# Kernel optimization log

Hardware: AMD Instinct MI355X
Metric: run time of the kernel (lower is better)

## Reference

```python
import jax, jax.numpy as jnp
import numpy as np

N, K, H = 50000, 8, 128  # nodes per level, mailbox fanout, hidden size


def setup_inputs() -> dict:
    key = jax.random.key(0)
    ks = jax.random.split(key, 16)
    s = 1.0 / np.sqrt(H)
    inp = {
        "x": jax.random.normal(ks[0], (N, H), jnp.float32),
        "h_mail": jax.random.normal(ks[1], (N, K, H), jnp.float32),
        "c_mail": jax.random.normal(ks[2], (N, K, H), jnp.float32),
        "Wiou": jax.random.uniform(ks[3], (H, 3 * H), jnp.float32, -s, s),
        "Uiou": jax.random.uniform(ks[4], (2 * H, 3 * H), jnp.float32, -s, s),
        "biou": jnp.zeros((1, 3 * H), jnp.float32),
        "Of": jax.random.uniform(ks[5], (H, H), jnp.float32, -s, s),
        "Zf": jax.random.uniform(ks[6], (H, H), jnp.float32, -s, s),
        "Qf": jax.random.uniform(ks[7], (H, H), jnp.float32, -s, s),
        "Kf": jax.random.uniform(ks[8], (H, H), jnp.float32, -s, s),
        "vf": jax.random.uniform(ks[9], (H, H), jnp.float32, -s, s),
        "Wa": jax.random.uniform(ks[10], (H, H), jnp.float32, -s, s),
        "Wd": jax.random.uniform(ks[11], (H, H), jnp.float32, -s, s),
        "Vf": jax.random.uniform(ks[12], (H, 1), jnp.float32, -s, s),
        "etype": jax.random.randint(ks[13], (N, K), 0, 2, jnp.int32),
    }
    return inp


def reference(x, h_mail, c_mail, Wiou, Uiou, biou, Of, Zf, Qf, Kf, vf, Wa, Wd, Vf, etype):
    # --- message: mailbox of child h, c and edge type e (0/1) ---
    e = etype.astype(x.dtype)[..., None]                     # [N,K,1]
    # --- reduce_func ---
    x_tild = x @ Wiou                                        # W_iou(features) -> iou  [N,3H]
    n_tild = x @ Qf                                          # [N,H]
    hk = h_mail @ Kf                                         # K_f(h_tild) [N,K,H]
    v_tild = hk @ vf                                         # [N,K,H]
    w = jax.nn.softmax(jnp.tanh((n_tild[:, None, :] + hk) @ Vf), axis=1)  # [N,K,1]
    modify = jnp.mean(e, axis=1)                             # sum(et)/K  [N,1]
    score_a = (1.0 - modify)[:, None, :]                     # [N,1,1]
    score_b = modify[:, None, :]
    h_til1 = jnp.sum(w * score_a * e * (v_tild @ Wa), axis=1)        # [N,H]
    h_til0 = jnp.sum(w * score_b * (1.0 - e) * (v_tild @ Wd), axis=1)
    h_tild = jnp.concatenate([h_til0, h_til1], axis=1)       # [N,2H]
    f = jax.nn.sigmoid((h_mail * e) @ Of + (h_mail * (1.0 - e)) @ Zf)
    c_red = jnp.sum(f * c_mail, axis=1)                      # [N,H]
    iou = h_tild @ Uiou + x_tild                             # [N,3H]
    # --- apply_node_func ---
    iou = iou + biou
    i, o, u = jnp.split(iou, 3, axis=1)
    i, o, u = jax.nn.sigmoid(i), jax.nn.sigmoid(o), jnp.tanh(u)
    c = i * u + c_red
    h = o * jnp.tanh(c)
    return jnp.stack([h, c])                                 # [2,N,H]
```

## Files before the change

kernel.cpp:

```cpp
#include <hip/hip_runtime.h>
#include <math.h>

#define NN 50000
#define HH 128
#define KK 8

#define WS_WTF  0
#define WS_BT   16384
#define WS_KV   90112
#define WS_T0   106496
#define WS_T1   122880
#define WS_kv   139264
#define WS_qv   139392

typedef __attribute__((ext_vector_type(8))) unsigned short u16x8;
typedef __attribute__((ext_vector_type(8))) __bf16 bf16x8;
typedef __attribute__((ext_vector_type(4))) float f32x4;
union Frag { u16x8 u; bf16x8 b; };

__device__ __forceinline__ unsigned short f2bf(float f) {
    unsigned u = __builtin_bit_cast(unsigned, f);
    u += 0x7fffu + ((u >> 16) & 1u);
    return (unsigned short)(u >> 16);
}
__device__ __forceinline__ float sigm(float v) { return 1.f / (1.f + expf(-v)); }

__global__ void prep1(const float* __restrict__ Kf, const float* __restrict__ Qf,
                      const float* __restrict__ vf, const float* __restrict__ Vf,
                      const float* __restrict__ Wiou, float* __restrict__ ws) {
    int idx = blockIdx.x * 256 + threadIdx.x;
    unsigned short* bt = (unsigned short*)(ws + WS_BT);
    if (idx < 16384) {
        int a = idx >> 7, c = idx & 127;
        float s = 0.f;
        for (int b = 0; b < 128; ++b) s += Kf[a * 128 + b] * vf[b * 128 + c];
        ws[WS_KV + idx] = s;
    } else if (idx < 16512) {
        int a = idx - 16384;
        float s = 0.f;
        for (int b = 0; b < 128; ++b) s += Kf[a * 128 + b] * Vf[b];
        ws[WS_kv + a] = s;
    } else if (idx < 16640) {
        int a = idx - 16512;
        float s = 0.f;
        for (int b = 0; b < 128; ++b) s += Qf[a * 128 + b] * Vf[b];
        ws[WS_qv + a] = s;
    } else {
        int i = idx - 16640;
        int r = i / 384, c = i % 384;
        bt[c * 384 + r] = f2bf(Wiou[i]);
    }
}

__global__ void prep2(const float* __restrict__ Wd, const float* __restrict__ Wa,
                      float* __restrict__ ws) {
    int idx = blockIdx.x * 256 + threadIdx.x;
    int sel = idx >> 14;
    int r = (idx >> 7) & 127, c = idx & 127;
    const float* W = sel ? Wa : Wd;
    const float* Kv = ws + WS_KV;
    float s = 0.f;
    for (int h = 0; h < 128; ++h) s += Kv[r * 128 + h] * W[h * 128 + c];
    ws[(sel ? WS_T1 : WS_T0) + r * 128 + c] = s;
}

__global__ void prep3(const float* __restrict__ Uiou, float* __restrict__ ws) {
    int idx = blockIdx.x * 256 + threadIdx.x;
    int half = (idx >= 49152) ? 1 : 0;
    int i2 = idx - half * 49152;
    int r = i2 / 384, c = i2 % 384;
    const float* T = ws + (half ? WS_T1 : WS_T0);
    const float* U = Uiou + half * 128 * 384;
    float s = 0.f;
    for (int h = 0; h < 128; ++h) s += T[r * 128 + h] * U[h * 384 + c];
    unsigned short* bt = (unsigned short*)(ws + WS_BT);
    bt[c * 384 + (128 + half * 128 + r)] = f2bf(s);
}

__global__ void prep4(const float* __restrict__ Of, const float* __restrict__ Zf,
                      float* __restrict__ ws) {
    int idx = blockIdx.x * 256 + threadIdx.x;
    int c = idx >> 8, k = idx & 255;
    float v = (k < 128) ? Of[k * 128 + c] : Zf[(k - 128) * 128 + c];
    unsigned short* wtf = (unsigned short*)(ws + WS_WTF);
    wtf[idx] = f2bf(v);
}

__global__ __launch_bounds__(256) void tree_main(
    const float* __restrict__ x, const float* __restrict__ h_mail,
    const float* __restrict__ c_mail, const float* __restrict__ biou,
    const int* __restrict__ etype, const float* __restrict__ ws,
    float* __restrict__ out)
{
    __shared__ unsigned short GfS[48 * 128];
    __shared__ float credS[16 * 128];
    __shared__ float iouS[16 * 388];
    __shared__ float efS[128];
    __shared__ float kvqS[256];

    const int t = threadIdx.x;
    const int node0 = blockIdx.x * 16;

    {
        const int n = t >> 4, s = t & 15, c0 = s * 8;
        const int node = node0 + n;
        kvqS[t] = ws[WS_kv + t];
        if (t < 128) efS[t] = (float)etype[node0 * KK + t];

        float xv[8];
        const float4* xp = (const float4*)(x + node * HH + c0);
        float4 x0 = xp[0], x1 = xp[1];
        xv[0]=x0.x; xv[1]=x0.y; xv[2]=x0.z; xv[3]=x0.w;
        xv[4]=x1.x; xv[5]=x1.y; xv[6]=x1.z; xv[7]=x1.w;
        u16x8 xg;
        #pragma unroll
        for (int j = 0; j < 8; ++j) xg[j] = f2bf(xv[j]);
        *(u16x8*)(&GfS[s * 128 + n * 8]) = xg;
        __syncthreads();

        float xq = 0.f;
        #pragma unroll
        for (int j = 0; j < 8; ++j) xq += xv[j] * kvqS[128 + c0 + j];

        float p[KK];
        #pragma unroll
        for (int k = 0; k < KK; ++k) {
            const float4* hp = (const float4*)(h_mail + (node * KK + k) * HH + c0);
            float4 h0 = hp[0], h1 = hp[1];
            p[k] = h0.x*kvqS[c0]   + h0.y*kvqS[c0+1] + h0.z*kvqS[c0+2] + h0.w*kvqS[c0+3]
                 + h1.x*kvqS[c0+4] + h1.y*kvqS[c0+5] + h1.z*kvqS[c0+6] + h1.w*kvqS[c0+7];
        }
        #pragma unroll
        for (int msk = 8; msk >= 1; msk >>= 1) {
            xq += __shfl_xor(xq, msk, 16);
            #pragma unroll
            for (int k = 0; k < KK; ++k) p[k] += __shfl_xor(p[k], msk, 16);
        }
        float ef[KK], esum = 0.f;
        #pragma unroll
        for (int k = 0; k < KK; ++k) { ef[k] = efS[n * KK + k]; esum += ef[k]; }
        const float mod = esum * 0.125f;
        const float sa = 1.f - mod, sb = mod;

        float tk[KK], mx = -1e30f;
        #pragma unroll
        for (int k = 0; k < KK; ++k) { tk[k] = tanhf(xq + p[k]); mx = fmaxf(mx, tk[k]); }
        float wsum = 0.f;
        #pragma unroll
        for (int k = 0; k < KK; ++k) { tk[k] = expf(tk[k] - mx); wsum += tk[k]; }
        const float inv = 1.f / wsum;
        float cf0[KK], cf1[KK];
        #pragma unroll
        for (int k = 0; k < KK; ++k) {
            float w = tk[k] * inv;
            cf0[k] = sb * w * (1.f - ef[k]);
            cf1[k] = sa * w * ef[k];
        }
        float a0[8] = {0,0,0,0,0,0,0,0}, a1[8] = {0,0,0,0,0,0,0,0};
        #pragma unroll
        for (int k = 0; k < KK; ++k) {
            const float4* hp = (const float4*)(h_mail + (node * KK + k) * HH + c0);
            float4 h0 = hp[0], h1 = hp[1];
            float hv[8];
            hv[0]=h0.x; hv[1]=h0.y; hv[2]=h0.z; hv[3]=h0.w;
            hv[4]=h1.x; hv[5]=h1.y; hv[6]=h1.z; hv[7]=h1.w;
            #pragma unroll
            for (int j = 0; j < 8; ++j) { a0[j] += cf0[k]*hv[j]; a1[j] += cf1[k]*hv[j]; }
        }
        u16x8 g0, g1;
        #pragma unroll
        for (int j = 0; j < 8; ++j) { g0[j] = f2bf(a0[j]); g1[j] = f2bf(a1[j]); }
        *(u16x8*)(&GfS[(16 + s) * 128 + n * 8]) = g0;
        *(u16x8*)(&GfS[(32 + s) * 128 + n * 8]) = g1;
    }
    __syncthreads();

    const int wave = t >> 6, lane = t & 63, m = lane & 15, q = lane >> 4;
    {
        const unsigned short* WtF = (const unsigned short*)(ws + WS_WTF);
        f32x4 acc[2][8];
        #pragma unroll
        for (int rt = 0; rt < 2; ++rt)
            #pragma unroll
            for (int tc = 0; tc < 8; ++tc) acc[rt][tc] = (f32x4){0.f,0.f,0.f,0.f};

        #pragma unroll
        for (int ks = 0; ks < 8; ++ks) {
            const int kg = ks * 32 + q * 8;
            Frag bf[8], af[2];
            #pragma unroll
            for (int tc = 0; tc < 8; ++tc)
                bf[tc].u = *(const u16x8*)(WtF + (tc * 16 + m) * 256 + kg);
            #pragma unroll
            for (int rt = 0; rt < 2; ++rt) {
                const int r = wave * 32 + rt * 16 + m;
                const float msk = (ks < 4) ? efS[r] : (1.f - efS[r]);
                const float4* hp = (const float4*)(h_mail + (node0 * KK + r) * HH + (kg & 127));
                float4 h0 = hp[0], h1 = hp[1];
                float tv[8];
                tv[0]=h0.x*msk; tv[1]=h0.y*msk; tv[2]=h0.z*msk; tv[3]=h0.w*msk;
                tv[4]=h1.x*msk; tv[5]=h1.y*msk; tv[6]=h1.z*msk; tv[7]=h1.w*msk;
                #pragma unroll
                for (int j = 0; j < 8; ++j) af[rt].u[j] = f2bf(tv[j]);
            }
            #pragma unroll
            for (int rt = 0; rt < 2; ++rt)
                #pragma unroll
                for (int tc = 0; tc < 8; ++tc)
                    acc[rt][tc] = __builtin_amdgcn_mfma_f32_16x16x32_bf16(
                        af[rt].b, bf[tc].b, acc[rt][tc], 0, 0, 0);
        }
        #pragma unroll
        for (int rt = 0; rt < 2; ++rt) {
            const int rbase = wave * 32 + rt * 16;
            #pragma unroll
            for (int tc = 0; tc < 8; ++tc) {
                float sacc = 0.f;
                #pragma unroll
                for (int reg = 0; reg < 4; ++reg) {
                    const int r = rbase + q * 4 + reg;
                    const float f = sigm(acc[rt][tc][reg]);
                    sacc += f * c_mail[(node0 * KK + r) * HH + tc * 16 + m];
                }
                sacc += __shfl_xor(sacc, 16);
                if ((q & 1) == 0) {
                    const int nl = (rbase >> 3) + (q >> 1);
                    credS[nl * 128 + tc * 16 + m] = sacc;
                }
            }
        }
    }

    {
        const unsigned short* Bt = (const unsigned short*)(ws + WS_BT);
        f32x4 acc2[6];
        #pragma unroll
        for (int j = 0; j < 6; ++j) acc2[j] = (f32x4){0.f,0.f,0.f,0.f};
        #pragma unroll
        for (int ks = 0; ks < 12; ++ks) {
            const int kg = ks * 32 + q * 8;
            Frag ag;
            ag.u = *(const u16x8*)(&GfS[(kg >> 3) * 128 + m * 8]);
            #pragma unroll
            for (int j = 0; j < 6; ++j) {
                const int tc = wave * 6 + j;
                Frag bg;
                bg.u = *(const u16x8*)(Bt + (tc * 16 + m) * 384 + kg);
                acc2[j] = __builtin_amdgcn_mfma_f32_16x16x32_bf16(
                    ag.b, bg.b, acc2[j], 0, 0, 0);
            }
        }
        #pragma unroll
        for (int j = 0; j < 6; ++j) {
            const int tc = wave * 6 + j;
            #pragma unroll
            for (int reg = 0; reg < 4; ++reg)
                iouS[(q * 4 + reg) * 388 + tc * 16 + m] = acc2[j][reg];
        }
    }
    __syncthreads();

    {
        const int n = t >> 4, s = t & 15, c0 = s * 8;
        const int node = node0 + n;
        float hb[8], cb[8];
        #pragma unroll
        for (int j = 0; j < 8; ++j) {
            const int c = c0 + j;
            const float ii = sigm(iouS[n * 388 + c] + biou[c]);
            const float oo = sigm(iouS[n * 388 + 128 + c] + biou[128 + c]);
            const float uu = tanhf(iouS[n * 388 + 256 + c] + biou[256 + c]);
            const float cc = ii * uu + credS[n * 128 + c];
            cb[j] = cc;
            hb[j] = oo * tanhf(cc);
        }
        float4* oh = (float4*)(out + node * HH + c0);
        oh[0] = make_float4(hb[0], hb[1], hb[2], hb[3]);
        oh[1] = make_float4(hb[4], hb[5], hb[6], hb[7]);
        float4* oc = (float4*)(out + NN * HH + node * HH + c0);
        oc[0] = make_float4(cb[0], cb[1], cb[2], cb[3]);
        oc[1] = make_float4(cb[4], cb[5], cb[6], cb[7]);
    }
}

extern "C" void kernel_launch(void* const* d_in, const int* in_sizes, int n_in,
                              void* d_out, int out_size, void* d_ws, size_t ws_size,
                              hipStream_t stream) {
    const float* x      = (const float*)d_in[0];
    const float* h_mail = (const float*)d_in[1];
    const float* c_mail = (const float*)d_in[2];
    const float* Uiou   = (const float*)d_in[4];
    const float* biou   = (const float*)d_in[5];
    const float* Of     = (const float*)d_in[6];
    const float* Zf     = (const float*)d_in[7];
    const float* Qf     = (const float*)d_in[8];
    const float* Kf     = (const float*)d_in[9];
    const float* vf     = (const float*)d_in[10];
    const float* Wa     = (const float*)d_in[11];
    const float* Wd     = (const float*)d_in[12];
    const float* Vf     = (const float*)d_in[13];
    const int*   etype  = (const int*)d_in[14];
    const float* Wiou   = (const float*)d_in[3];
    float* ws  = (float*)d_ws;
    float* out = (float*)d_out;

    hipLaunchKernelGGL(prep1, dim3(257), dim3(256), 0, stream, Kf, Qf, vf, Vf, Wiou, ws);
    hipLaunchKernelGGL(prep2, dim3(128), dim3(256), 0, stream, Wd, Wa, ws);
    hipLaunchKernelGGL(prep3, dim3(384), dim3(256), 0, stream, Uiou, ws);
    hipLaunchKernelGGL(prep4, dim3(128), dim3(256), 0, stream, Of, Zf, ws);
    hipLaunchKernelGGL(tree_main, dim3(3125), dim3(256), 0, stream,
                       x, h_mail, c_mail, biou, etype, ws, out);
}
```

Baseline: 745.9 us.

## Fuse prep kernels, cache h_mail rows, and apply gates straight from MFMA registers

Merges the Of/Zf transpose into the first prep kernel, removing one launch. In the main kernel, h_mail values are kept in registers between the score pass and the weighted-sum pass, so they are not reloaded. The c_mail loads are hoisted ahead of the sigmoid-multiply loop. The iou MFMA tile mapping is changed so each wave holds matching i/o/u columns, which lets the gate math run directly from the accumulators without the iouS shared buffer. It also adds launch_bounds occupancy 4 and pads credS. The trade-off is higher register pressure from hv[8][8] and cm[8][4] under the occupancy cap, which may cause spills, and output stores become scalar instead of float4.

```diff
diff --git a/kernel.cpp b/kernel.cpp
--- a/kernel.cpp
+++ b/kernel.cpp
@@ -25,9 +25,10 @@
 }
 __device__ __forceinline__ float sigm(float v) { return 1.f / (1.f + expf(-v)); }
 
-__global__ void prep1(const float* __restrict__ Kf, const float* __restrict__ Qf,
+__global__ void prepA(const float* __restrict__ Kf, const float* __restrict__ Qf,
                       const float* __restrict__ vf, const float* __restrict__ Vf,
-                      const float* __restrict__ Wiou, float* __restrict__ ws) {
+                      const float* __restrict__ Wiou, const float* __restrict__ Of,
+                      const float* __restrict__ Zf, float* __restrict__ ws) {
     int idx = blockIdx.x * 256 + threadIdx.x;
     unsigned short* bt = (unsigned short*)(ws + WS_BT);
     if (idx < 16384) {
@@ -45,10 +46,16 @@
         float s = 0.f;
         for (int b = 0; b < 128; ++b) s += Qf[a * 128 + b] * Vf[b];
         ws[WS_qv + a] = s;
-    } else {
+    } else if (idx < 65792) {
         int i = idx - 16640;
         int r = i / 384, c = i % 384;
         bt[c * 384 + r] = f2bf(Wiou[i]);
+    } else {
+        int i = idx - 65792;
+        int c = i >> 8, k = i & 255;
+        float v = (k < 128) ? Of[k * 128 + c] : Zf[(k - 128) * 128 + c];
+        unsigned short* wtf = (unsigned short*)(ws + WS_WTF);
+        wtf[i] = f2bf(v);
     }
 }
 
@@ -77,24 +84,14 @@
     bt[c * 384 + (128 + half * 128 + r)] = f2bf(s);
 }
 
-__global__ void prep4(const float* __restrict__ Of, const float* __restrict__ Zf,
-                      float* __restrict__ ws) {
-    int idx = blockIdx.x * 256 + threadIdx.x;
-    int c = idx >> 8, k = idx & 255;
-    float v = (k < 128) ? Of[k * 128 + c] : Zf[(k - 128) * 128 + c];
-    unsigned short* wtf = (unsigned short*)(ws + WS_WTF);
-    wtf[idx] = f2bf(v);
-}
-
-__global__ __launch_bounds__(256) void tree_main(
+__global__ __launch_bounds__(256, 4) void tree_main(
     const float* __restrict__ x, const float* __restrict__ h_mail,
     const float* __restrict__ c_mail, const float* __restrict__ biou,
     const int* __restrict__ etype, const float* __restrict__ ws,
     float* __restrict__ out)
 {
     __shared__ unsigned short GfS[48 * 128];
-    __shared__ float credS[16 * 128];
-    __shared__ float iouS[16 * 388];
+    __shared__ float credS[16 * 132];
     __shared__ float efS[128];
     __shared__ float kvqS[256];
 
@@ -122,13 +119,18 @@
         #pragma unroll
         for (int j = 0; j < 8; ++j) xq += xv[j] * kvqS[128 + c0 + j];
 
+        float hv[KK][8];
         float p[KK];
         #pragma unroll
         for (int k = 0; k < KK; ++k) {
             const float4* hp = (const float4*)(h_mail + (node * KK + k) * HH + c0);
             float4 h0 = hp[0], h1 = hp[1];
-            p[k] = h0.x*kvqS[c0]   + h0.y*kvqS[c0+1] + h0.z*kvqS[c0+2] + h0.w*kvqS[c0+3]
-                 + h1.x*kvqS[c0+4] + h1.y*kvqS[c0+5] + h1.z*kvqS[c0+6] + h1.w*kvqS[c0+7];
+            hv[k][0]=h0.x; hv[k][1]=h0.y; hv[k][2]=h0.z; hv[k][3]=h0.w;
+            hv[k][4]=h1.x; hv[k][5]=h1.y; hv[k][6]=h1.z; hv[k][7]=h1.w;
+            float pk = 0.f;
+            #pragma unroll
+            for (int j = 0; j < 8; ++j) pk += hv[k][j] * kvqS[c0 + j];
+            p[k] = pk;
         }
         #pragma unroll
         for (int msk = 8; msk >= 1; msk >>= 1) {
@@ -149,23 +151,14 @@
         #pragma unroll
         for (int k = 0; k < KK; ++k) { tk[k] = expf(tk[k] - mx); wsum += tk[k]; }
         const float inv = 1.f / wsum;
-        float cf0[KK], cf1[KK];
+        float a0[8] = {0,0,0,0,0,0,0,0}, a1[8] = {0,0,0,0,0,0,0,0};
         #pragma unroll
         for (int k = 0; k < KK; ++k) {
             float w = tk[k] * inv;
-            cf0[k] = sb * w * (1.f - ef[k]);
-            cf1[k] = sa * w * ef[k];
-        }
-        float a0[8] = {0,0,0,0,0,0,0,0}, a1[8] = {0,0,0,0,0,0,0,0};
-        #pragma unroll
-        for (int k = 0; k < KK; ++k) {
-            const float4* hp = (const float4*)(h_mail + (node * KK + k) * HH + c0);
-            float4 h0 = hp[0], h1 = hp[1];
-            float hv[8];
-            hv[0]=h0.x; hv[1]=h0.y; hv[2]=h0.z; hv[3]=h0.w;
-            hv[4]=h1.x; hv[5]=h1.y; hv[6]=h1.z; hv[7]=h1.w;
-            #pragma unroll
-            for (int j = 0; j < 8; ++j) { a0[j] += cf0[k]*hv[j]; a1[j] += cf1[k]*hv[j]; }
+            const float cf0 = sb * w * (1.f - ef[k]);
+            const float cf1 = sa * w * ef[k];
+            #pragma unroll
+            for (int j = 0; j < 8; ++j) { a0[j] += cf0 * hv[k][j]; a1[j] += cf1 * hv[k][j]; }
         }
         u16x8 g0, g1;
         #pragma unroll
@@ -213,27 +206,31 @@
         #pragma unroll
         for (int rt = 0; rt < 2; ++rt) {
             const int rbase = wave * 32 + rt * 16;
+            const float* cp = c_mail + (node0 * KK + rbase + q * 4) * HH + m;
+            float cm[8][4];
+            #pragma unroll
+            for (int tc = 0; tc < 8; ++tc)
+                #pragma unroll
+                for (int reg = 0; reg < 4; ++reg)
+                    cm[tc][reg] = cp[reg * HH + tc * 16];
             #pragma unroll
             for (int tc = 0; tc < 8; ++tc) {
                 float sacc = 0.f;
                 #pragma unroll
-                for (int reg = 0; reg < 4; ++reg) {
-                    const int r = rbase + q * 4 + reg;
-                    const float f = sigm(acc[rt][tc][reg]);
-                    sacc += f * c_mail[(node0 * KK + r) * HH + tc * 16 + m];
-                }
+                for (int reg = 0; reg < 4; ++reg)
+                    sacc += sigm(acc[rt][tc][reg]) * cm[tc][reg];
                 sacc += __shfl_xor(sacc, 16);
                 if ((q & 1) == 0) {
                     const int nl = (rbase >> 3) + (q >> 1);
-                    credS[nl * 128 + tc * 16 + m] = sacc;
+                    credS[nl * 132 + tc * 16 + m] = sacc;
                 }
             }
         }
     }
 
+    f32x4 acc2[6];
     {
         const unsigned short* Bt = (const unsigned short*)(ws + WS_BT);
-        f32x4 acc2[6];
         #pragma unroll
         for (int j = 0; j < 6; ++j) acc2[j] = (f32x4){0.f,0.f,0.f,0.f};
         #pragma unroll
@@ -243,43 +240,34 @@
             ag.u = *(const u16x8*)(&GfS[(kg >> 3) * 128 + m * 8]);
             #pragma unroll
             for (int j = 0; j < 6; ++j) {
-                const int tc = wave * 6 + j;
+                const int tile = (j >> 1) * 8 + wave * 2 + (j & 1);
                 Frag bg;
-                bg.u = *(const u16x8*)(Bt + (tc * 16 + m) * 384 + kg);
+                bg.u = *(const u16x8*)(Bt + (tile * 16 + m) * 384 + kg);
                 acc2[j] = __builtin_amdgcn_mfma_f32_16x16x32_bf16(
                     ag.b, bg.b, acc2[j], 0, 0, 0);
             }
         }
-        #pragma unroll
-        for (int j = 0; j < 6; ++j) {
-            const int tc = wave * 6 + j;
-            #pragma unroll
-            for (int reg = 0; reg < 4; ++reg)
-                iouS[(q * 4 + reg) * 388 + tc * 16 + m] = acc2[j][reg];
-        }
     }
     __syncthreads();
 
     {
-        const int n = t >> 4, s = t & 15, c0 = s * 8;
-        const int node = node0 + n;
-        float hb[8], cb[8];
-        #pragma unroll
-        for (int j = 0; j < 8; ++j) {
-            const int c = c0 + j;
-            const float ii = sigm(iouS[n * 388 + c] + biou[c]);
-            const float oo = sigm(iouS[n * 388 + 128 + c] + biou[128 + c]);
-            const float uu = tanhf(iouS[n * 388 + 256 + c] + biou[256 + c]);
-            const float cc = ii * uu + credS[n * 128 + c];
-            cb[j] = cc;
-            hb[j] = oo * tanhf(cc);
-        }
-        float4* oh = (float4*)(out + node * HH + c0);
-        oh[0] = make_float4(hb[0], hb[1], hb[2], hb[3]);
-        oh[1] = make_float4(hb[4], hb[5], hb[6], hb[7]);
-        float4* oc = (float4*)(out + NN * HH + node * HH + c0);
-        oc[0] = make_float4(cb[0], cb[1], cb[2], cb[3]);
-        oc[1] = make_float4(cb[4], cb[5], cb[6], cb[7]);
+        #pragma unroll
+        for (int jj = 0; jj < 2; ++jj) {
+            const int c = (wave * 2 + jj) * 16 + m;
+            const float bi = biou[c];
+            const float bo = biou[128 + c];
+            const float bu = biou[256 + c];
+            #pragma unroll
+            for (int reg = 0; reg < 4; ++reg) {
+                const int n = q * 4 + reg;
+                const float ii = sigm(acc2[jj][reg] + bi);
+                const float oo = sigm(acc2[2 + jj][reg] + bo);
+                const float uu = tanhf(acc2[4 + jj][reg] + bu);
+                const float cc = ii * uu + credS[n * 132 + c];
+                out[(node0 + n) * HH + c] = oo * tanhf(cc);
+                out[NN * HH + (node0 + n) * HH + c] = cc;
+            }
+        }
     }
 }
 
@@ -304,10 +292,9 @@
     float* ws  = (float*)d_ws;
     float* out = (float*)d_out;
 
-    hipLaunchKernelGGL(prep1, dim3(257), dim3(256), 0, stream, Kf, Qf, vf, Vf, Wiou, ws);
+    hipLaunchKernelGGL(prepA, dim3(385), dim3(256), 0, stream, Kf, Qf, vf, Vf, Wiou, Of, Zf, ws);
     hipLaunchKernelGGL(prep2, dim3(128), dim3(256), 0, stream, Wd, Wa, ws);
     hipLaunchKernelGGL(prep3, dim3(384), dim3(256), 0, stream, Uiou, ws);
-    hipLaunchKernelGGL(prep4, dim3(128), dim3(256), 0, stream, Of, Zf, ws);
     hipLaunchKernelGGL(tree_main, dim3(3125), dim3(256), 0, stream,
                        x, h_mail, c_mail, biou, etype, ws, out);
 }
```

Result: slower. 847.7 us (+13.7%).
